# Performance work log

Hardware: AMD Instinct MI355X
Metric: run time of the kernel (lower is better)

Reference implementation:

```python
import jax, jax.numpy as jnp
import numpy as np
import math

EMBED_DIM = 256
NUM_HEADS = 8
FFN_DIM = 1024
EPS = 1e-5


def layer_norm(x, g, b):
    mu = jnp.mean(x, axis=-1, keepdims=True)
    var = jnp.var(x, axis=-1, keepdims=True)
    return (x - mu) / jnp.sqrt(var + EPS) * g + b


def setup_inputs() -> dict:
    key = jax.random.key(0)
    ks = jax.random.split(key, 10)
    B, L, D, F = 4, 2048, EMBED_DIM, FFN_DIM
    x = jax.random.normal(ks[0], (B, L, D), dtype=jnp.float32)
    mask = jnp.ones((B, L), dtype=jnp.int32)
    # FFN params (PyTorch Linear default-ish scale)
    W1 = jax.random.normal(ks[1], (D, F), dtype=jnp.float32) / np.sqrt(D)
    b1 = jnp.zeros((F,), dtype=jnp.float32)
    W2 = jax.random.normal(ks[2], (F, D), dtype=jnp.float32) / np.sqrt(F)
    b2 = jnp.zeros((D,), dtype=jnp.float32)
    g1 = jnp.ones((D,), dtype=jnp.float32)
    be1 = jnp.zeros((D,), dtype=jnp.float32)
    g2 = jnp.ones((D,), dtype=jnp.float32)
    be2 = jnp.zeros((D,), dtype=jnp.float32)
    return {"x": x, "mask": mask, "W1": W1, "b1": b1, "W2": W2, "b2": b2,
            "g1": g1, "be1": be1, "g2": g2, "be2": be2}


def quantum_attention(x, mask):
    B, L, D = x.shape
    H, dk = NUM_HEADS, D // NUM_HEADS
    xh = x.reshape(B, L, H, dk).transpose(0, 2, 1, 3)  # [B,H,L,dk]
    # per-token mean over batch and heads -> [L, dk]
    m = jnp.mean(xh, axis=(0, 1))
    # closed form of the single-qubit RX circuit: P(|1>) = sin^2(angle/2)
    dot = m @ m.T  # [L, L]
    ang = jnp.clip(dot, -math.pi, math.pi)
    scores = jnp.sin(ang * 0.5) ** 2  # [L, L], shared across B and H
    attn = jnp.broadcast_to(scores[None, None], (B, H, L, L))
    attn = jnp.where(mask[:, None, None, :] == 0, -1e9, attn)
    attn = jax.nn.softmax(attn, axis=-1)
    out = jnp.einsum('bhij,bhjd->bhid', attn, xh)  # values are xh itself
    return out.transpose(0, 2, 1, 3).reshape(B, L, D)


def reference(x, mask, W1, b1, W2, b2, g1, be1, g2, be2):
    attn_out = quantum_attention(x, mask)
    h = layer_norm(x + attn_out, g1, be1)
    ffn = jax.nn.relu(h @ W1 + b1) @ W2 + b2
    return layer_norm(h + ffn, g2, be2)
```

## Files before the change

kernel.cpp:

```cpp
#include <hip/hip_runtime.h>
#include <hip/hip_bf16.h>


#define B_ 4
#define L_ 2048
#define D_ 256
#define F_ 1024
#define PI_F 3.14159265358979323846f

typedef __bf16 bf16x8 __attribute__((ext_vector_type(8)));
typedef float floatx4 __attribute__((ext_vector_type(4)));
typedef unsigned short ushortx4 __attribute__((ext_vector_type(4)));
typedef unsigned short ushortx8 __attribute__((ext_vector_type(8)));

#define WAIT_VM(n) asm volatile("s_waitcnt vmcnt(" #n ")" ::: "memory")
#define WAIT_LGKM() asm volatile("s_waitcnt lgkmcnt(0)" ::: "memory")
#define SCHED0() __builtin_amdgcn_sched_barrier(0)
#define BARRIER() do { SCHED0(); __builtin_amdgcn_s_barrier(); SCHED0(); } while (0)

__device__ __forceinline__ unsigned short f2bf(float f) {
    unsigned int u = __float_as_uint(f);
    u = (u + 0x7FFFu + ((u >> 16) & 1u)) >> 16;
    return (unsigned short)u;
}
__device__ __forceinline__ float bf2f(unsigned short u) {
    union { unsigned int i; float f; } v; v.i = ((unsigned int)u) << 16; return v.f;
}

__device__ __forceinline__ void async_cp16(unsigned short* lds, const unsigned short* g) {
    __builtin_amdgcn_global_load_lds(
        (const __attribute__((address_space(1))) unsigned int*)g,
        (__attribute__((address_space(3))) unsigned int*)lds, 16, 0, 0);
}

__global__ __launch_bounds__(256) void k_prep(const float* __restrict__ x,
                                              const float* __restrict__ W1,
                                              const float* __restrict__ W2,
                                              const int* __restrict__ mask,
                                              unsigned short* __restrict__ mb,
                                              unsigned short* __restrict__ XmT,
                                              unsigned short* __restrict__ W1T,
                                              unsigned short* __restrict__ W2T) {
    __shared__ float tile[32][33];
    int r = blockIdx.x, t = threadIdx.x;
    if (r >= 2560) {
        if (r < 2816) {
            int idx = (r - 2560) * 256 + t;
            int l = idx >> 5, k = idx & 31;
            float s = 0.f;
#pragma unroll
            for (int b = 0; b < B_; b++) {
                const float* xp = x + ((size_t)(b * L_ + l)) * D_ + k;
#pragma unroll
                for (int h = 0; h < 8; h++) s += xp[h * 32];
            }
            mb[idx] = f2bf(s * (1.f / 32.f));
        } else {
#pragma unroll
            for (int c = 0; c < 32; c++) {
                int e = c * 256 + t;
                int b = e >> 11, j = e & (L_ - 1);
                XmT[(size_t)(1024 + b) * L_ + j] = mask[b * L_ + j] ? 0x3F80 : 0;
            }
        }
        return;
    }
    const float* in; unsigned short* outp; int R, C; const int* mrow = nullptr; size_t bo = 0;
    int bx, by;
    if (r < 2048) {
        int z = r >> 9, rem = r & 511; by = rem >> 3; bx = rem & 7;
        in = x; outp = XmT; R = L_; C = 256; bo = (size_t)z * R * C; mrow = mask + z * L_;
    } else if (r < 2304) {
        int rem = r - 2048; bx = rem & 31; by = rem >> 5;
        in = W1; outp = W1T; R = 256; C = 1024;
    } else {
        int rem = r - 2304; bx = rem & 7; by = rem >> 3;
        in = W2; outp = W2T; R = 1024; C = 256;
    }
    int r0 = by * 32, c0 = bx * 32;
    int tx = t & 31, ty = t >> 5;
#pragma unroll
    for (int rr = 0; rr < 4; rr++) {
        int rw = ty + rr * 8;
        tile[rw][tx] = in[bo + (size_t)(r0 + rw) * C + c0 + tx];
    }
    float mfac = 1.f;
    if (mrow) mfac = mrow[r0 + tx] ? 1.f : 0.f;
    __syncthreads();
#pragma unroll
    for (int rr = 0; rr < 4; rr++) {
        int c = ty + rr * 8;
        outp[bo + (size_t)(c0 + c) * R + r0 + tx] = f2bf(tile[tx][c] * mfac);
    }
}

__global__ __launch_bounds__(256) void k_scores_mfma(const unsigned short* __restrict__ mb,
                                                     unsigned short* __restrict__ E) {
    const int t = threadIdx.x, lane = t & 63, wid = t >> 6;
    const int wm = (wid >> 1) * 64, wn = (wid & 1) * 32;
    const int lr = lane & 15, lq = lane >> 4;
    int m0 = blockIdx.y * 128, n0 = blockIdx.x * 64;
    bf16x8 af[4], bfr[2];
#pragma unroll
    for (int i = 0; i < 4; i++)
        af[i] = *(const bf16x8*)(mb + (size_t)(m0 + wm + i * 16 + lr) * 32 + lq * 8);
#pragma unroll
    for (int j = 0; j < 2; j++)
        bfr[j] = *(const bf16x8*)(mb + (size_t)(n0 + wn + j * 16 + lr) * 32 + lq * 8);
    floatx4 acc[4][2];
#pragma unroll
    for (int i = 0; i < 4; i++)
#pragma unroll
        for (int j = 0; j < 2; j++) {
            acc[i][j] = (floatx4){0.f, 0.f, 0.f, 0.f};
            acc[i][j] = __builtin_amdgcn_mfma_f32_16x16x32_bf16(af[i], bfr[j], acc[i][j], 0, 0, 0);
        }
#pragma unroll
    for (int i = 0; i < 4; i++)
#pragma unroll
        for (int j = 0; j < 2; j++)
#pragma unroll
            for (int r = 0; r < 4; r++) {
                int row = m0 + wm + i * 16 + lq * 4 + r;
                int col = n0 + wn + j * 16 + lr;
                float d = fminf(fmaxf(acc[i][j][r], -PI_F), PI_F);
                float sn = __sinf(0.5f * d);
                E[(size_t)row * L_ + col] = f2bf(__expf(sn * sn));
            }
}

__global__ __launch_bounds__(256) void k_av(const unsigned short* __restrict__ E,
                                            const unsigned short* __restrict__ XmT,
                                            unsigned short* __restrict__ Cb,
                                            float* __restrict__ rs) {
    __shared__ __align__(16) unsigned short sbuf[3][128 * 64 + 64 * 64 + 16 * 64];
    const int t = threadIdx.x, lane = t & 63, wid = t >> 6;
    const int wm = (wid >> 1) * 64, wn = (wid & 1) * 32;
    const int lr = lane & 15, lq = lane >> 4;
    const int lrow = lane >> 3, lseg = lane & 7;

    int bid = blockIdx.x;
    int swz = (bid & 7) * 32 + (bid >> 3);
    int m0 = (swz >> 4) * 128, n0 = (swz & 15) * 64;
    const bool doMask = (n0 == 0);
    const bool maskw = doMask && ((wid & 1) == 0);

    const unsigned short* Ag[4]; int sAoff[4];
#pragma unroll
    for (int q = 0; q < 4; q++) {
        int rl = wid * 32 + q * 8 + lrow;
        Ag[q] = E + (size_t)(m0 + rl) * L_ + ((lseg - rl) & 7) * 8;
        sAoff[q] = (wid * 32 + q * 8) * 64;
    }
    const unsigned short* Bg[2]; int sBoff[2];
#pragma unroll
    for (int q = 0; q < 2; q++) {
        int rl = wid * 16 + q * 8 + lrow;
        Bg[q] = XmT + (size_t)(n0 + rl) * L_ + ((lseg - rl) & 7) * 8;
        sBoff[q] = 8192 + (wid * 16 + q * 8) * 64;
    }
    const unsigned short* Mg = XmT + (size_t)(1024 + wid) * L_ + (((lane - wid) & 7) * 8);
    const int sMoff = 12288 + wid * 64;

    int arot[4], aroff[4], brot[2], broff[2];
#pragma unroll
    for (int i = 0; i < 4; i++) { int ar = wm + i * 16 + lr; aroff[i] = ar * 64; arot[i] = lq + ar; }
#pragma unroll
    for (int j = 0; j < 2; j++) { int br = wn + j * 16 + lr; broff[j] = 8192 + br * 64; brot[j] = lq + br; }
    const int mroff = 12288 + lr * 64, mrot = lq + lr;

    floatx4 acc[4][2], acc3[4];
#pragma unroll
    for (int i = 0; i < 4; i++) {
#pragma unroll
        for (int j = 0; j < 2; j++) acc[i][j] = (floatx4){0.f, 0.f, 0.f, 0.f};
        acc3[i] = (floatx4){0.f, 0.f, 0.f, 0.f};
    }

    auto stage = [&](unsigned short* base, int k0) {
#pragma unroll
        for (int q = 0; q < 4; q++) async_cp16(base + sAoff[q], Ag[q] + k0);
#pragma unroll
        for (int q = 0; q < 2; q++) async_cp16(base + sBoff[q], Bg[q] + k0);
    };
    auto stageM = [&](unsigned short* base, int k0) {
        if (lane < 8) async_cp16(base + sMoff, Mg + k0);
    };
    auto compute = [&](const unsigned short* base) {
#pragma unroll
        for (int s = 0; s < 2; s++) {
            bf16x8 af[4], bfr[2];
#pragma unroll
            for (int i = 0; i < 4; i++)
                af[i] = *(const bf16x8*)(base + aroff[i] + ((s * 4 + arot[i]) & 7) * 8);
#pragma unroll
            for (int j = 0; j < 2; j++)
                bfr[j] = *(const bf16x8*)(base + broff[j] + ((s * 4 + brot[j]) & 7) * 8);
#pragma unroll
            for (int i = 0; i < 4; i++)
#pragma unroll
                for (int j = 0; j < 2; j++)
                    acc[i][j] = __builtin_amdgcn_mfma_f32_16x16x32_bf16(af[i], bfr[j], acc[i][j], 0, 0, 0);
            if (maskw) {
                bf16x8 bm = *(const bf16x8*)(base + mroff + ((s * 4 + mrot) & 7) * 8);
#pragma unroll
                for (int i = 0; i < 4; i++)
                    acc3[i] = __builtin_amdgcn_mfma_f32_16x16x32_bf16(af[i], bm, acc3[i], 0, 0, 0);
            }
        }
    };

    unsigned short *p0 = sbuf[0], *p1 = sbuf[1], *p2 = sbuf[2];
    if (doMask) {
        stage(p0, 0); stageM(p0, 0); stage(p1, 64); stageM(p1, 64); stage(p2, 128); stageM(p2, 128);
        WAIT_VM(14); BARRIER();
        for (int p = 0; p < 29; ++p) {
            compute(p0);
            BARRIER();
            stage(p0, (p + 3) << 6); stageM(p0, (p + 3) << 6);
            WAIT_VM(14); BARRIER();
            unsigned short* tmp = p0; p0 = p1; p1 = p2; p2 = tmp;
        }
        compute(p0); BARRIER();
        WAIT_VM(7); BARRIER();
        compute(p1); BARRIER();
        WAIT_VM(0); BARRIER();
        compute(p2);
    } else {
        stage(p0, 0); stage(p1, 64); stage(p2, 128);
        WAIT_VM(12); BARRIER();
        for (int p = 0; p < 29; ++p) {
            compute(p0);
            BARRIER();
            stage(p0, (p + 3) << 6);
            WAIT_VM(12); BARRIER();
            unsigned short* tmp = p0; p0 = p1; p1 = p2; p2 = tmp;
        }
        compute(p0); BARRIER();
        WAIT_VM(6); BARRIER();
        compute(p1); BARRIER();
        WAIT_VM(0); BARRIER();
        compute(p2);
    }

#pragma unroll
    for (int i = 0; i < 4; i++)
#pragma unroll
        for (int j = 0; j < 2; j++)
#pragma unroll
            for (int r = 0; r < 4; r++) {
                int row = m0 + wm + i * 16 + lq * 4 + r;
                int col = n0 + wn + j * 16 + lr;
                Cb[(size_t)row * 1024 + col] = f2bf(acc[i][j][r]);
            }
    if (maskw && lr < 4) {
#pragma unroll
        for (int i = 0; i < 4; i++)
#pragma unroll
            for (int r = 0; r < 4; r++) {
                int row = m0 + wm + i * 16 + lq * 4 + r;
                rs[(size_t)row * 4 + lr] = acc3[i][r];
            }
    }
}

__global__ __launch_bounds__(512, 1) void k_ffn(const float* __restrict__ x,
                                                const unsigned short* __restrict__ Cb,
                                                const float* __restrict__ rs,
                                                const unsigned short* __restrict__ W1T,
                                                const unsigned short* __restrict__ W2T,
                                                const float* __restrict__ b1,
                                                const float* __restrict__ b2,
                                                const float* __restrict__ g1, const float* __restrict__ be1,
                                                const float* __restrict__ g2, const float* __restrict__ be2,
                                                float* __restrict__ out) {
    __shared__ __align__(16) unsigned short hA[4 * 32 * 64];
    __shared__ __align__(16) unsigned short W1b[2][4 * 64 * 64];
    __shared__ __align__(16) unsigned short W2b[2][4 * 64 * 64];
    __shared__ __align__(16) unsigned short t1c[2][32 * 72];
    __shared__ float b1s[1024];
    __shared__ float red[4][32][2];

    const int t = threadIdx.x, lane = t & 63, wid = t >> 6;
    const bool isG1 = wid < 4;
    const int gw = wid & 3;
    const int lr = lane & 15, lq = lane >> 4;
    const int half = lane >> 5, l32 = lane & 31;
    const int lrow8 = lane >> 3, kk = lane & 7;
    const int m0 = blockIdx.x * 32;

    auto stageW1 = [&](unsigned short* buf, int fc) {
#pragma unroll
        for (int q = 0; q < 8; q++) {
            int kc = q >> 1, sub = q & 1;
            int fl = sub * 32 + gw * 8 + lrow8;
            const unsigned short* src = W1T + (size_t)(fc * 64 + fl) * 256 + kc * 64 + (((kk - fl) & 7) * 8);
            async_cp16(buf + kc * 4096 + sub * 2048 + gw * 512, src);
        }
    };
    auto stageW2 = [&](unsigned short* buf, int fc) {
#pragma unroll
        for (int q = 0; q < 8; q++) {
            int nc = q >> 1, sub = q & 1;
            int nl = sub * 32 + gw * 8 + lrow8;
            const unsigned short* src = W2T + (size_t)(nc * 64 + nl) * 1024 + fc * 64 + (((kk - nl) & 7) * 8);
            async_cp16(buf + nc * 4096 + sub * 2048 + gw * 512, src);
        }
    };

    if (isG1) { stageW1(W1b[0], 0); stageW1(W1b[1], 1); }
    else      { stageW2(W2b[0], 0); stageW2(W2b[1], 1); }

    b1s[t] = b1[t];
    b1s[512 + t] = b1[512 + t];
    float4 g1a = *(const float4*)(g1 + l32 * 8);
    float4 g1b = *(const float4*)(g1 + l32 * 8 + 4);
    float4 be1a = *(const float4*)(be1 + l32 * 8);
    float4 be1b = *(const float4*)(be1 + l32 * 8 + 4);

#pragma unroll
    for (int it = 0; it < 2; it++) {
        int tloc = wid * 4 + it * 2 + half;
        int tok = m0 + tloc;
        int bi = tok >> 11, ii = tok & (L_ - 1);
        float rsv = rs[(size_t)ii * 4 + bi];
        float4 xv0 = *(const float4*)(x + (size_t)tok * D_ + l32 * 8);
        float4 xv1 = *(const float4*)(x + (size_t)tok * D_ + l32 * 8 + 4);
        ushortx8 cv = *(const ushortx8*)(Cb + (size_t)ii * 1024 + bi * 256 + l32 * 8);
        float v[8];
        v[0] = xv0.x + bf2f(cv[0]) / rsv; v[1] = xv0.y + bf2f(cv[1]) / rsv;
        v[2] = xv0.z + bf2f(cv[2]) / rsv; v[3] = xv0.w + bf2f(cv[3]) / rsv;
        v[4] = xv1.x + bf2f(cv[4]) / rsv; v[5] = xv1.y + bf2f(cv[5]) / rsv;
        v[6] = xv1.z + bf2f(cv[6]) / rsv; v[7] = xv1.w + bf2f(cv[7]) / rsv;
        float s = 0.f, s2 = 0.f;
#pragma unroll
        for (int k = 0; k < 8; k++) { s += v[k]; s2 += v[k] * v[k]; }
#pragma unroll
        for (int o = 1; o < 32; o <<= 1) { s += __shfl_xor(s, o); s2 += __shfl_xor(s2, o); }
        float mu = s * (1.f / 256.f);
        float var = s2 * (1.f / 256.f) - mu * mu;
        float rq = rsqrtf(var + 1e-5f);
        union { bf16x8 v8; unsigned short u[8]; } hv;
        hv.u[0] = f2bf((v[0] - mu) * rq * g1a.x + be1a.x);
        hv.u[1] = f2bf((v[1] - mu) * rq * g1a.y + be1a.y);
        hv.u[2] = f2bf((v[2] - mu) * rq * g1a.z + be1a.z);
        hv.u[3] = f2bf((v[3] - mu) * rq * g1a.w + be1a.w);
        hv.u[4] = f2bf((v[4] - mu) * rq * g1b.x + be1b.x);
        hv.u[5] = f2bf((v[5] - mu) * rq * g1b.y + be1b.y);
        hv.u[6] = f2bf((v[6] - mu) * rq * g1b.z + be1b.z);
        hv.u[7] = f2bf((v[7] - mu) * rq * g1b.w + be1b.w);
        *(bf16x8*)(hA + (l32 >> 3) * 2048 + tloc * 64 + ((((l32 & 7) + tloc) & 7) * 8)) = hv.v8;
    }
    WAIT_VM(0); WAIT_LGKM(); BARRIER();

    bf16x8 haf[2][8];
    if (isG1) {
#pragma unroll
        for (int i = 0; i < 2; i++)
#pragma unroll
            for (int kc = 0; kc < 4; kc++)
#pragma unroll
                for (int s = 0; s < 2; s++) {
                    int row = i * 16 + lr;
                    haf[i][kc * 2 + s] = *(const bf16x8*)(hA + kc * 2048 + row * 64 + (((s * 4 + lq + row) & 7) * 8));
                }
    }

    floatx4 acc[2][4];
#pragma unroll
    for (int i = 0; i < 2; i++)
#pragma unroll
        for (int j = 0; j < 4; j++) acc[i][j] = (floatx4){0.f, 0.f, 0.f, 0.f};

    const int wcol = gw * 16 + lr;

#pragma unroll 1
    for (int cc = 0; cc <= 16; ++cc) {
        if (cc >= 15) { WAIT_VM(0); } else { WAIT_VM(8); }
        BARRIER();
        if (isG1) {
            if (cc < 16) {
                const unsigned short* w1cur = W1b[cc & 1];
                floatx4 a1[2] = { (floatx4){0.f,0.f,0.f,0.f}, (floatx4){0.f,0.f,0.f,0.f} };
#pragma unroll
                for (int kc = 0; kc < 4; kc++)
#pragma unroll
                    for (int s = 0; s < 2; s++) {
                        bf16x8 bfr = *(const bf16x8*)(w1cur + kc * 4096 + wcol * 64 + (((s * 4 + lq + wcol) & 7) * 8));
                        a1[0] = __builtin_amdgcn_mfma_f32_16x16x32_bf16(haf[0][kc * 2 + s], bfr, a1[0], 0, 0, 0);
                        a1[1] = __builtin_amdgcn_mfma_f32_16x16x32_bf16(haf[1][kc * 2 + s], bfr, a1[1], 0, 0, 0);
                    }
                float bv = b1s[cc * 64 + wcol];
                unsigned short* tc = t1c[cc & 1];
#pragma unroll
                for (int i = 0; i < 2; i++)
#pragma unroll
                    for (int r = 0; r < 4; r++)
                        tc[(i * 16 + lq * 4 + r) * 72 + wcol] = f2bf(fmaxf(a1[i][r] + bv, 0.f));
                WAIT_LGKM();
            }
        } else {
            if (cc >= 1) {
                int d = cc - 1;
                const unsigned short* w2cur = W2b[d & 1];
                const unsigned short* tc = t1c[d & 1];
#pragma unroll
                for (int s = 0; s < 2; s++) {
                    bf16x8 af0 = *(const bf16x8*)(tc + lr * 72 + s * 32 + lq * 8);
                    bf16x8 af1 = *(const bf16x8*)(tc + (16 + lr) * 72 + s * 32 + lq * 8);
#pragma unroll
                    for (int j = 0; j < 4; j++) {
                        int nl = j * 16 + lr;
                        bf16x8 bfr = *(const bf16x8*)(w2cur + gw * 4096 + nl * 64 + (((s * 4 + lq + nl) & 7) * 8));
                        acc[0][j] = __builtin_amdgcn_mfma_f32_16x16x32_bf16(af0, bfr, acc[0][j], 0, 0, 0);
                        acc[1][j] = __builtin_amdgcn_mfma_f32_16x16x32_bf16(af1, bfr, acc[1][j], 0, 0, 0);
                    }
                }
            }
        }
        BARRIER();
        if (isG1) {
            if (cc <= 13) stageW1(W1b[cc & 1], cc + 2);
        } else {
            if (cc >= 1 && cc <= 14) stageW2(W2b[(cc - 1) & 1], cc + 1);
        }
    }

    float psum[2][4], psq[2][4];
#pragma unroll
    for (int i = 0; i < 2; i++)
#pragma unroll
        for (int r = 0; r < 4; r++) { psum[i][r] = 0.f; psq[i][r] = 0.f; }
    if (!isG1) {
#pragma unroll
        for (int i = 0; i < 2; i++)
#pragma unroll
            for (int j = 0; j < 4; j++) {
                int col = gw * 64 + j * 16 + lr;
                float bv = b2[col];
                int kc = col >> 6, ks = (col >> 3) & 7, ke = col & 7;
#pragma unroll
                for (int r = 0; r < 4; r++) {
                    int row = i * 16 + lq * 4 + r;
                    float hres = bf2f(hA[kc * 2048 + row * 64 + (((ks + row) & 7) * 8) + ke]);
                    float v = acc[i][j][r] + bv + hres;
                    acc[i][j][r] = v;
                    psum[i][r] += v; psq[i][r] += v * v;
                }
            }
#pragma unroll
        for (int o = 1; o < 16; o <<= 1)
#pragma unroll
            for (int i = 0; i < 2; i++)
#pragma unroll
                for (int r = 0; r < 4; r++) { psum[i][r] += __shfl_xor(psum[i][r], o); psq[i][r] += __shfl_xor(psq[i][r], o); }
        if (lr == 0) {
#pragma unroll
            for (int i = 0; i < 2; i++)
#pragma unroll
                for (int r = 0; r < 4; r++) {
                    int lrow = i * 16 + lq * 4 + r;
                    red[gw][lrow][0] = psum[i][r];
                    red[gw][lrow][1] = psq[i][r];
                }
        }
    }
    __syncthreads();
    if (!isG1) {
#pragma unroll
        for (int i = 0; i < 2; i++)
#pragma unroll
            for (int r = 0; r < 4; r++) {
                int lrow = i * 16 + lq * 4 + r;
                float s  = red[0][lrow][0] + red[1][lrow][0] + red[2][lrow][0] + red[3][lrow][0];
                float s2 = red[0][lrow][1] + red[1][lrow][1] + red[2][lrow][1] + red[3][lrow][1];
                float mu = s * (1.f / 256.f);
                float var = s2 * (1.f / 256.f) - mu * mu;
                float rc = rsqrtf(var + 1e-5f);
                int row = m0 + lrow;
#pragma unroll
                for (int j = 0; j < 4; j++) {
                    int col = gw * 64 + j * 16 + lr;
                    out[(size_t)row * 256 + col] = (acc[i][j][r] - mu) * rc * g2[col] + be2[col];
                }
            }
    }
}

extern "C" void kernel_launch(void* const* d_in, const int* in_sizes, int n_in,
                              void* d_out, int out_size, void* d_ws, size_t ws_size,
                              hipStream_t stream) {
    const float* x   = (const float*)d_in[0];
    const int*  mask = (const int*)d_in[1];
    const float* W1  = (const float*)d_in[2];
    const float* b1  = (const float*)d_in[3];
    const float* W2  = (const float*)d_in[4];
    const float* b2  = (const float*)d_in[5];
    const float* g1  = (const float*)d_in[6];
    const float* be1 = (const float*)d_in[7];
    const float* g2  = (const float*)d_in[8];
    const float* be2 = (const float*)d_in[9];
    float* out = (float*)d_out;

    char* w = (char*)d_ws;
    unsigned short* mb_   = (unsigned short*)w;  w += 65536 * 2;
    unsigned short* E_    = (unsigned short*)w;  w += (size_t)L_ * L_ * 2;
    unsigned short* XmT_  = (unsigned short*)w;  w += (size_t)1088 * L_ * 2;
    unsigned short* W1T_  = (unsigned short*)w;  w += 262144 * 2;
    unsigned short* W2T_  = (unsigned short*)w;  w += 262144 * 2;
    unsigned short* Cb_   = (unsigned short*)w;  w += (size_t)L_ * 1024 * 2;
    float*          rs_   = (float*)w;           w += (size_t)L_ * 4 * 4;

    k_prep<<<2817, 256, 0, stream>>>(x, W1, W2, mask, mb_, XmT_, W1T_, W2T_);
    k_scores_mfma<<<dim3(32, 16), 256, 0, stream>>>(mb_, E_);
    k_av<<<256, 256, 0, stream>>>(E_, XmT_, Cb_, rs_);
    k_ffn<<<256, 512, 0, stream>>>(x, Cb_, rs_, W1T_, W2T_, b1, b2, g1, be1, g2, be2, out);
}
```

Measured before the change: 133.9 us.

## Use 8 waves per block in k_av with smaller per-wave tiles

The attention-value GEMM kernel moves from 256 to 512 threads per block. Each wave now computes a 32x32 sub-tile instead of 64x32, and the global-to-LDS staging is spread across twice as many waves. The separate masked and unmasked pipelines merge into one loop with conditional wait counts. The aim is more latency hiding and MFMA issue parallelism per CU for the 256-block grid, at the cost of less register-level reuse per wave and more LDS fragment reads per MFMA.

```diff
diff --git a/kernel.cpp b/kernel.cpp
--- a/kernel.cpp
+++ b/kernel.cpp
@@ -129,13 +129,13 @@
             }
 }
 
-__global__ __launch_bounds__(256) void k_av(const unsigned short* __restrict__ E,
+__global__ __launch_bounds__(512) void k_av(const unsigned short* __restrict__ E,
                                             const unsigned short* __restrict__ XmT,
                                             unsigned short* __restrict__ Cb,
                                             float* __restrict__ rs) {
     __shared__ __align__(16) unsigned short sbuf[3][128 * 64 + 64 * 64 + 16 * 64];
     const int t = threadIdx.x, lane = t & 63, wid = t >> 6;
-    const int wm = (wid >> 1) * 64, wn = (wid & 1) * 32;
+    const int wm3 = (wid >> 1) * 32, wn3 = (wid & 1) * 32;
     const int lr = lane & 15, lq = lane >> 4;
     const int lrow = lane >> 3, lseg = lane & 7;
 
@@ -144,34 +144,35 @@
     int m0 = (swz >> 4) * 128, n0 = (swz & 15) * 64;
     const bool doMask = (n0 == 0);
     const bool maskw = doMask && ((wid & 1) == 0);
-
-    const unsigned short* Ag[4]; int sAoff[4];
-#pragma unroll
-    for (int q = 0; q < 4; q++) {
-        int rl = wid * 32 + q * 8 + lrow;
-        Ag[q] = E + (size_t)(m0 + rl) * L_ + ((lseg - rl) & 7) * 8;
-        sAoff[q] = (wid * 32 + q * 8) * 64;
-    }
-    const unsigned short* Bg[2]; int sBoff[2];
+    const bool mload = doMask && (wid < 4);
+
+    const unsigned short* Ag[2]; int sAoff[2];
 #pragma unroll
     for (int q = 0; q < 2; q++) {
         int rl = wid * 16 + q * 8 + lrow;
-        Bg[q] = XmT + (size_t)(n0 + rl) * L_ + ((lseg - rl) & 7) * 8;
-        sBoff[q] = 8192 + (wid * 16 + q * 8) * 64;
+        Ag[q] = E + (size_t)(m0 + rl) * L_ + ((lseg - rl) & 7) * 8;
+        sAoff[q] = (wid * 16 + q * 8) * 64;
+    }
+    const unsigned short* Bg;
+    int sBoff;
+    {
+        int rl = wid * 8 + lrow;
+        Bg = XmT + (size_t)(n0 + rl) * L_ + ((lseg - rl) & 7) * 8;
+        sBoff = 8192 + (wid * 8) * 64;
     }
     const unsigned short* Mg = XmT + (size_t)(1024 + wid) * L_ + (((lane - wid) & 7) * 8);
     const int sMoff = 12288 + wid * 64;
 
-    int arot[4], aroff[4], brot[2], broff[2];
-#pragma unroll
-    for (int i = 0; i < 4; i++) { int ar = wm + i * 16 + lr; aroff[i] = ar * 64; arot[i] = lq + ar; }
-#pragma unroll
-    for (int j = 0; j < 2; j++) { int br = wn + j * 16 + lr; broff[j] = 8192 + br * 64; brot[j] = lq + br; }
+    int arot[2], aroff[2], brot[2], broff[2];
+#pragma unroll
+    for (int i = 0; i < 2; i++) { int ar = wm3 + i * 16 + lr; aroff[i] = ar * 64; arot[i] = lq + ar; }
+#pragma unroll
+    for (int j = 0; j < 2; j++) { int br = wn3 + j * 16 + lr; broff[j] = 8192 + br * 64; brot[j] = lq + br; }
     const int mroff = 12288 + lr * 64, mrot = lq + lr;
 
-    floatx4 acc[4][2], acc3[4];
-#pragma unroll
-    for (int i = 0; i < 4; i++) {
+    floatx4 acc[2][2], acc3[2];
+#pragma unroll
+    for (int i = 0; i < 2; i++) {
 #pragma unroll
         for (int j = 0; j < 2; j++) acc[i][j] = (floatx4){0.f, 0.f, 0.f, 0.f};
         acc3[i] = (floatx4){0.f, 0.f, 0.f, 0.f};
@@ -179,86 +180,69 @@
 
     auto stage = [&](unsigned short* base, int k0) {
 #pragma unroll
-        for (int q = 0; q < 4; q++) async_cp16(base + sAoff[q], Ag[q] + k0);
-#pragma unroll
-        for (int q = 0; q < 2; q++) async_cp16(base + sBoff[q], Bg[q] + k0);
-    };
-    auto stageM = [&](unsigned short* base, int k0) {
-        if (lane < 8) async_cp16(base + sMoff, Mg + k0);
+        for (int q = 0; q < 2; q++) async_cp16(base + sAoff[q], Ag[q] + k0);
+        async_cp16(base + sBoff, Bg + k0);
+        if (mload && lane < 8) async_cp16(base + sMoff, Mg + k0);
     };
     auto compute = [&](const unsigned short* base) {
 #pragma unroll
         for (int s = 0; s < 2; s++) {
-            bf16x8 af[4], bfr[2];
-#pragma unroll
-            for (int i = 0; i < 4; i++)
+            bf16x8 af[2], bfr[2];
+#pragma unroll
+            for (int i = 0; i < 2; i++)
                 af[i] = *(const bf16x8*)(base + aroff[i] + ((s * 4 + arot[i]) & 7) * 8);
 #pragma unroll
             for (int j = 0; j < 2; j++)
                 bfr[j] = *(const bf16x8*)(base + broff[j] + ((s * 4 + brot[j]) & 7) * 8);
 #pragma unroll
-            for (int i = 0; i < 4; i++)
+            for (int i = 0; i < 2; i++)
 #pragma unroll
                 for (int j = 0; j < 2; j++)
                     acc[i][j] = __builtin_amdgcn_mfma_f32_16x16x32_bf16(af[i], bfr[j], acc[i][j], 0, 0, 0);
             if (maskw) {
                 bf16x8 bm = *(const bf16x8*)(base + mroff + ((s * 4 + mrot) & 7) * 8);
 #pragma unroll
-                for (int i = 0; i < 4; i++)
+                for (int i = 0; i < 2; i++)
                     acc3[i] = __builtin_amdgcn_mfma_f32_16x16x32_bf16(af[i], bm, acc3[i], 0, 0, 0);
             }
         }
     };
 
     unsigned short *p0 = sbuf[0], *p1 = sbuf[1], *p2 = sbuf[2];
-    if (doMask) {
-        stage(p0, 0); stageM(p0, 0); stage(p1, 64); stageM(p1, 64); stage(p2, 128); stageM(p2, 128);
-        WAIT_VM(14); BARRIER();
-        for (int p = 0; p < 29; ++p) {
-            compute(p0);
-            BARRIER();
-            stage(p0, (p + 3) << 6); stageM(p0, (p + 3) << 6);
-            WAIT_VM(14); BARRIER();
-            unsigned short* tmp = p0; p0 = p1; p1 = p2; p2 = tmp;
-        }
-        compute(p0); BARRIER();
-        WAIT_VM(7); BARRIER();
-        compute(p1); BARRIER();
-        WAIT_VM(0); BARRIER();
-        compute(p2);
-    } else {
-        stage(p0, 0); stage(p1, 64); stage(p2, 128);
-        WAIT_VM(12); BARRIER();
-        for (int p = 0; p < 29; ++p) {
-            compute(p0);
-            BARRIER();
-            stage(p0, (p + 3) << 6);
-            WAIT_VM(12); BARRIER();
-            unsigned short* tmp = p0; p0 = p1; p1 = p2; p2 = tmp;
-        }
-        compute(p0); BARRIER();
-        WAIT_VM(6); BARRIER();
-        compute(p1); BARRIER();
-        WAIT_VM(0); BARRIER();
-        compute(p2);
-    }
-
-#pragma unroll
-    for (int i = 0; i < 4; i++)
+    stage(p0, 0); stage(p1, 64); stage(p2, 128);
+    if (mload) { WAIT_VM(8); } else { WAIT_VM(6); }
+    BARRIER();
+    for (int p = 0; p < 29; ++p) {
+        compute(p0);
+        BARRIER();
+        stage(p0, (p + 3) << 6);
+        if (mload) { WAIT_VM(8); } else { WAIT_VM(6); }
+        BARRIER();
+        unsigned short* tmp = p0; p0 = p1; p1 = p2; p2 = tmp;
+    }
+    compute(p0); BARRIER();
+    if (mload) { WAIT_VM(4); } else { WAIT_VM(3); }
+    BARRIER();
+    compute(p1); BARRIER();
+    WAIT_VM(0); BARRIER();
+    compute(p2);
+
+#pragma unroll
+    for (int i = 0; i < 2; i++)
 #pragma unroll
         for (int j = 0; j < 2; j++)
 #pragma unroll
             for (int r = 0; r < 4; r++) {
-                int row = m0 + wm + i * 16 + lq * 4 + r;
-                int col = n0 + wn + j * 16 + lr;
+                int row = m0 + wm3 + i * 16 + lq * 4 + r;
+                int col = n0 + wn3 + j * 16 + lr;
                 Cb[(size_t)row * 1024 + col] = f2bf(acc[i][j][r]);
             }
     if (maskw && lr < 4) {
 #pragma unroll
-        for (int i = 0; i < 4; i++)
+        for (int i = 0; i < 2; i++)
 #pragma unroll
             for (int r = 0; r < 4; r++) {
-                int row = m0 + wm + i * 16 + lq * 4 + r;
+                int row = m0 + wm3 + i * 16 + lq * 4 + r;
                 rs[(size_t)row * 4 + lr] = acc3[i][r];
             }
     }
@@ -513,6 +497,6 @@
 
     k_prep<<<2817, 256, 0, stream>>>(x, W1, W2, mask, mb_, XmT_, W1T_, W2T_);
     k_scores_mfma<<<dim3(32, 16), 256, 0, stream>>>(mb_, E_);
-    k_av<<<256, 256, 0, stream>>>(E_, XmT_, Cb_, rs_);
+    k_av<<<256, 512, 0, stream>>>(E_, XmT_, Cb_, rs_);
     k_ffn<<<256, 512, 0, stream>>>(x, Cb_, rs_, W1T_, W2T_, b1, b2, g1, be1, g2, be2, out);
 }
```

Measured after the change: 131.7 us. No clear change (-1.7%).
